# Kernel tuning notes

Measured on AMD Instinct MI355X. Metric: run time of the kernel, lower is better.

The kernel has to match this reference:

```python
import jax, jax.numpy as jnp
import numpy as np

B, L, N, C = 32, 12, 512, 2
UNITS, OUT_DIM, HORIZON, K, NUM_LAYERS = 64, 1, 12, 2, 2
M = 2 * K + 1  # 2 supports * K diffusion steps + identity


def _random_walk(adj):
    # adj: (B, N, N); D^-1 (adj + I)
    adj = adj + jnp.eye(adj.shape[1], dtype=adj.dtype)[None]
    d_inv = 1.0 / jnp.sum(adj, axis=2)
    d_inv = jnp.where(jnp.isinf(d_inv), 0.0, d_inv)
    return d_inv[:, :, None] * adj  # diag(d_inv) @ adj


def _gconv(x_in, state, supports, W, b):
    # x_in: (B, N*in), state: (B, N*units) -> (B, N*out)
    b_sz = x_in.shape[0]
    x = jnp.concatenate([x_in.reshape(b_sz, N, -1), state.reshape(b_sz, N, -1)], axis=2)
    f = x.shape[2]
    x0 = x
    xs = [x0]
    for A in supports:
        x1 = jnp.einsum('bij,bjf->bif', A, x0)
        xs.append(x1)
        for _ in range(2, K + 1):
            x2 = 2.0 * jnp.einsum('bij,bjf->bif', A, x1) - x0
            xs.append(x2)
            x1, x0 = x2, x1  # faithful to original code (x0 carries across supports)
    xcat = jnp.stack(xs, axis=0)              # (M, B, N, f)
    xcat = xcat.transpose(1, 2, 3, 0).reshape(b_sz * N, f * M)
    out = xcat @ W + b
    return out.reshape(b_sz, N * W.shape[1])


def _cell(inp, hx, supports, p):
    Wg, bg, Wc, bc = p
    gate = jax.nn.sigmoid(_gconv(inp, hx, supports, Wg, bg)).reshape(-1, N, 2 * UNITS)
    r = gate[..., :UNITS].reshape(-1, N * UNITS)
    u = gate[..., UNITS:].reshape(-1, N * UNITS)
    c = jnp.tanh(_gconv(inp, r * hx, supports, Wc, bc))
    return u * hx + (1.0 - u) * c


def setup_inputs() -> dict:
    key = jax.random.key(0)
    ks = iter(jax.random.split(key, 32))
    def nrm(shape, scale=0.1):
        return jax.random.normal(next(ks), shape, dtype=jnp.float32) * scale
    inp = {
        'history_data': jax.random.normal(next(ks), (B, L, N, C), dtype=jnp.float32),
        'hidden_states': jax.random.normal(next(ks), (B, N, 96), dtype=jnp.float32),
        'sampled_adj': jax.random.uniform(next(ks), (B, N, N), dtype=jnp.float32),
    }
    sizes = {'enc0': C + UNITS, 'enc1': 2 * UNITS, 'dec0': OUT_DIM + UNITS, 'dec1': 2 * UNITS}
    for name, isz in sizes.items():
        inp[name + '_Wg'] = nrm((isz * M, 2 * UNITS))
        inp[name + '_bg'] = jnp.ones((2 * UNITS,), jnp.float32)   # bias_start=1.0
        inp[name + '_Wc'] = nrm((isz * M, UNITS))
        inp[name + '_bc'] = jnp.zeros((UNITS,), jnp.float32)
    inp['proj_W'] = nrm((UNITS, OUT_DIM))
    inp['proj_b'] = jnp.zeros((OUT_DIM,), jnp.float32)
    inp['fc1_W'] = nrm((96, 256))
    inp['fc1_b'] = jnp.zeros((256,), jnp.float32)
    inp['fc2_W'] = nrm((256, 64))
    inp['fc2_b'] = jnp.zeros((64,), jnp.float32)
    return inp


def _forward(history_data, hidden_states, sampled_adj,
             enc0_Wg, enc0_bg, enc0_Wc, enc0_bc, enc1_Wg, enc1_bg, enc1_Wc, enc1_bc,
             dec0_Wg, dec0_bg, dec0_Wc, dec0_bc, dec1_Wg, dec1_bg, dec1_Wc, dec1_bc,
             proj_W, proj_b, fc1_W, fc1_b, fc2_W, fc2_b):
    supports = [_random_walk(sampled_adj), _random_walk(jnp.swapaxes(sampled_adj, -1, -2))]
    enc_params = [(enc0_Wg, enc0_bg, enc0_Wc, enc0_bc), (enc1_Wg, enc1_bg, enc1_Wc, enc1_bc)]
    dec_params = [(dec0_Wg, dec0_bg, dec0_Wc, dec0_bc), (dec1_Wg, dec1_bg, dec1_Wc, dec1_bc)]

    hist = jnp.transpose(history_data.reshape(B, L, N * C), (1, 0, 2))  # (L, B, N*C)

    def enc_step(h, x_t):
        out = x_t
        new_h = []
        for i, p in enumerate(enc_params):
            nh = _cell(out, h[i], supports, p)
            new_h.append(nh)
            out = nh
        return jnp.stack(new_h), None

    h0 = jnp.zeros((NUM_LAYERS, B, N * UNITS), dtype=hist.dtype)
    enc_h, _ = jax.lax.scan(enc_step, h0, hist)

    # fc_his on TSFormer hidden states, added to every encoder layer's hidden
    his = jax.nn.relu(jax.nn.relu(hidden_states @ fc1_W + fc1_b) @ fc2_W + fc2_b)  # (B, N, 64)
    enc_h = (enc_h.reshape(NUM_LAYERS, B, N, UNITS) + his[None]).reshape(NUM_LAYERS, B, N * UNITS)

    go = jnp.zeros((B, N * OUT_DIM), dtype=hist.dtype)

    def dec_step(carry, _):
        dec_in, h = carry
        out = dec_in
        new_h = []
        for i, p in enumerate(dec_params):
            nh = _cell(out, h[i], supports, p)
            new_h.append(nh)
            out = nh
        proj = (out.reshape(-1, UNITS) @ proj_W + proj_b).reshape(B, N * OUT_DIM)
        return (proj, jnp.stack(new_h)), proj

    _, outs = jax.lax.scan(dec_step, (go, enc_h), None, length=HORIZON)  # (L, B, N*OUT)
    return jnp.transpose(outs, (1, 2, 0))  # (B, N*OUT_DIM, HORIZON)


def reference(history_data, hidden_states, sampled_adj,
              enc0_Wg, enc0_bg, enc0_Wc, enc0_bc, enc1_Wg, enc1_bg, enc1_Wc, enc1_bc,
              dec0_Wg, dec0_bg, dec0_Wc, dec0_bc, dec1_Wg, dec1_bg, dec1_Wc, dec1_bc,
              proj_W, proj_b, fc1_W, fc1_b, fc2_W, fc2_b):
    return _forward(history_data, hidden_states, sampled_adj,
                    enc0_Wg, enc0_bg, enc0_Wc, enc0_bc, enc1_Wg, enc1_bg, enc1_Wc, enc1_bc,
                    dec0_Wg, dec0_bg, dec0_Wc, dec0_bc, dec1_Wg, dec1_bg, dec1_Wc, dec1_bc,
                    proj_W, proj_b, fc1_W, fc1_b, fc2_W, fc2_b)
```

## Files before the change

kernel.cpp:

```cpp
#include <hip/hip_runtime.h>
#include <stdint.h>
#include <string.h>
#include <math.h>


using bfrag = __attribute__((__ext_vector_type__(8))) short;
using accv  = __attribute__((__ext_vector_type__(4))) float;

#define DEVI static __device__ __forceinline__

DEVI float bf2f(short x) {
  union { unsigned u; float f; } v; v.u = ((unsigned)(unsigned short)x) << 16; return v.f;
}
DEVI short f2bf(float f) {
  union { float f; unsigned u; } v; v.f = f;
  unsigned r = v.u + 0x7FFFu + ((v.u >> 16) & 1u);
  return (short)(r >> 16);
}
DEVI float ldx(const void* p, long i, int f32) {
  return f32 ? ((const float*)p)[i] : bf2f(((const short*)p)[i]);
}
DEVI void gl16(const short* g, short* l) {
  __builtin_amdgcn_global_load_lds(
      (const __attribute__((address_space(1))) void*)g,
      (__attribute__((address_space(3))) void*)l, 16, 0, 0);
}
template<int N> DEVI void s_wait_vmcnt() {
  asm volatile("s_waitcnt vmcnt(%0)" :: "i"(N) : "memory");
}

struct GP {
  const short* A;  long sA;  int lda;
  const short* BT; long sBT; int ldbt;
  int K;
  short* C; long sC; int ldc;
  short* CT;
  const void* bias;
  const short* V0;
  const int* flg;
  int outDim, oshift;
  int mtiles;
  const float* h; float* hw; const float* u;
  short* xc; int inpOff;
  const short* wct; short* vtcout;
  short* xgs; int xgsOff;
  short* xch;
  short* nxg; short* nxc;
  const void* hsrc; long hoff;
  const void* prw; const void* prb; void* dout; int tstep;
  short* xo0; short* xo1;
};

template<int EPI, int BM, int BN, int BK, int THR, int SWZ, int PIPE, int PAIR = 0>
__global__ __launch_bounds__(THR)
void gemm_k(GP pa, GP pb) {
  constexpr int W    = THR / 64;
  constexpr int WROW = BM / 32;
  constexpr int WCOL = (W / WROW < 1) ? 1 : W / WROW;
  constexpr int NT   = BN / (16 * WCOL);
  constexpr int CH   = BK / 8;
  constexpr int AI   = (BM * CH) / THR;
  constexpr int BI   = (BN * CH) / THR;
  constexpr int LD   = AI + BI;
  constexpr int TB   = (BM + BN) * BK;
  __shared__ __align__(16) short lds[PIPE*TB];
  const int tid  = threadIdx.x;
  const int w    = tid >> 6;
  const int lane = tid & 63;
  const int quad = lane >> 4, l16 = lane & 15;
  const int rowW = (w % WROW) * 32;
  const int colW = (w / WROW) * (NT * 16);
  int lay = 0;
  if constexpr (PAIR) lay = blockIdx.z;
  const GP& p = lay ? pb : pa;
  int m0, n0, bz;
  if constexpr (SWZ == 1) {
    const int blk = blockIdx.x;
    bz = blk & 31;
    const int tile = blk >> 5;
    if (EPI == 4 && p.wct != nullptr && BN == 64) {
      m0 = (tile >> 1) * BM; n0 = (tile & 1) * BN;
    } else {
      m0 = (tile % p.mtiles) * BM;
      n0 = (tile / p.mtiles) * BN;
    }
  } else {
    m0 = blockIdx.x * BM; n0 = blockIdx.y * BN;
    bz = PAIR ? 0 : blockIdx.z;
  }

  const short* Ab = p.A  + (long)bz * p.sA + m0 * (long)p.lda;
  const short* Bb = p.BT + (long)bz * p.sBT + n0 * (long)p.ldbt;

  accv acc[2][NT];
#pragma unroll
  for (int i = 0; i < 2; i++)
#pragma unroll
    for (int j = 0; j < NT; j++) { accv z = {0.f,0.f,0.f,0.f}; acc[i][j] = z; }

  const short* asrc[AI]; int aoff[AI];
#pragma unroll
  for (int i = 0; i < AI; i++) {
    const int s = (w*AI + i)*64 + lane;
    const int r = s / CH, c = (s % CH) ^ (r & 7);
    asrc[i] = Ab + (long)r * p.lda + c*8;
    aoff[i] = (w*AI + i)*512;
  }
  const short* bsrc[BI]; int boff[BI];
#pragma unroll
  for (int i = 0; i < BI; i++) {
    const int s = (w*BI + i)*64 + lane;
    const int r = s / CH, c = (s % CH) ^ (r & 7);
    bsrc[i] = Bb + (long)r * p.ldbt + c*8;
    boff[i] = BM*BK + (w*BI + i)*512;
  }

  const int nIter = p.K / BK;
#pragma unroll
  for (int s = 0; s < PIPE-1; ++s) {
    if (s < nIter) {
      const int kk = s * BK;
#pragma unroll
      for (int i = 0; i < AI; i++) gl16(asrc[i] + kk, &lds[s*TB + aoff[i]]);
#pragma unroll
      for (int i = 0; i < BI; i++) gl16(bsrc[i] + kk, &lds[s*TB + boff[i]]);
    }
  }

  for (int it = 0; it < nIter; ++it) {
    const int bufO = (it & (PIPE-1)) * TB;
    if (it + PIPE - 1 < nIter) {
      const int nxt = ((it + PIPE - 1) & (PIPE-1)) * TB;
      const int kk = (it + PIPE - 1) * BK;
#pragma unroll
      for (int i = 0; i < AI; i++) gl16(asrc[i] + kk, &lds[nxt + aoff[i]]);
#pragma unroll
      for (int i = 0; i < BI; i++) gl16(bsrc[i] + kk, &lds[nxt + boff[i]]);
    }
    const int rem = nIter - 1 - it;
    if (rem >= PIPE-1) { s_wait_vmcnt<(PIPE-1)*LD>(); }
    else {
      if constexpr (PIPE >= 8) { if (rem == 6) s_wait_vmcnt<6*LD>(); }
      if constexpr (PIPE >= 7) { if (rem == 5) s_wait_vmcnt<5*LD>(); }
      if constexpr (PIPE >= 6) { if (rem == 4) s_wait_vmcnt<4*LD>(); }
      if constexpr (PIPE >= 5) { if (rem == 3) s_wait_vmcnt<3*LD>(); }
      if constexpr (PIPE >= 4) { if (rem == 2) s_wait_vmcnt<2*LD>(); }
      if (rem == 1) s_wait_vmcnt<1*LD>();
      else if (rem == 0) s_wait_vmcnt<0>();
    }
    asm volatile("s_barrier" ::: "memory");
#pragma unroll
    for (int ks = 0; ks < BK; ks += 32) {
      const int ch = (ks >> 3) + quad;
      bfrag fa[2];
#pragma unroll
      for (int rt = 0; rt < 2; rt++) {
        const int ar = rowW + rt*16 + l16;
        fa[rt] = *(const bfrag*)&lds[bufO + (ar*CH + (ch ^ (ar & 7))) * 8];
      }
#pragma unroll
      for (int nt = 0; nt < NT; nt++) {
        const int br = colW + nt*16 + l16;
        bfrag fb = *(const bfrag*)&lds[bufO + BM*BK + (br*CH + (ch ^ (br & 7))) * 8];
        acc[0][nt] = __builtin_amdgcn_mfma_f32_16x16x32_bf16(fa[0], fb, acc[0][nt], 0, 0, 0);
        acc[1][nt] = __builtin_amdgcn_mfma_f32_16x16x32_bf16(fa[1], fb, acc[1][nt], 0, 0, 0);
      }
    }
    asm volatile("s_barrier" ::: "memory");
  }

  int f32 = 0;
  if constexpr (EPI == 1 || EPI == 4 || EPI == 5) f32 = *p.flg;

  if constexpr (EPI == 0 || EPI == 1 || EPI == 2) {
#pragma unroll
    for (int rt = 0; rt < 2; rt++) {
      const int rbase = m0 + rowW + rt*16 + quad*4;
#pragma unroll
      for (int nt = 0; nt < NT; nt++) {
        const int cc = n0 + colW + nt*16 + l16;
#pragma unroll
        for (int e = 0; e < 4; e++) {
          float val = acc[rt][nt][e];
          if constexpr (EPI == 1) { val += ldx(p.bias, cc, f32); val = val > 0.f ? val : 0.f; }
          p.C[(long)bz * p.sC + (long)(rbase + e) * p.ldc + cc] = f2bf(val);
        }
      }
    }
  }
  if constexpr (EPI == 2 || EPI == 3) {
    __syncthreads();
#pragma unroll
    for (int rt = 0; rt < 2; rt++)
#pragma unroll
      for (int nt = 0; nt < NT; nt++)
#pragma unroll
        for (int e = 0; e < 4; e++)
          lds[(colW + nt*16 + l16)*136 + (rowW + rt*16 + quad*4 + e)] = f2bf(acc[rt][nt][e]);
    __syncthreads();
    const int c = tid >> 2, seg = tid & 3;
    const int cG = n0 + c;
    const short* sp = &lds[c*136 + seg*32];
    long dst;
    if constexpr (EPI == 3) {
      const int m  = cG >> p.oshift;
      const int o  = cG & (p.outDim - 1);
      const int bb = m0 >> 9;
      dst = ((long)((bb * p.outDim + o) * 5 + m) << 9) + (m0 & 511) + seg*32;
    } else {
      dst = (((long)bz << 9) + cG) * 512 + m0 + seg*32;
    }
    short* dp = p.CT + dst;
    *(bfrag*)(dp)      = *(const bfrag*)(sp);
    *(bfrag*)(dp + 8)  = *(const bfrag*)(sp + 8);
    *(bfrag*)(dp + 16) = *(const bfrag*)(sp + 16);
    *(bfrag*)(dp + 24) = *(const bfrag*)(sp + 24);
  }
  if constexpr (EPI == 4) {
#pragma unroll
    for (int rt = 0; rt < 2; rt++) {
      const int nb = m0 + rowW + rt*16 + quad*4;
#pragma unroll
      for (int nt = 0; nt < NT; nt++) {
        const int o = n0 + colW + nt*16 + l16;
        const float bv = ldx(p.bias, o, f32);
#pragma unroll
        for (int e = 0; e < 4; e++) {
          const int nn = nb + e;
          float val = acc[rt][nt][e] + bv +
                      bf2f(p.V0[(long)(bz * p.outDim + o) * 2560 + nn]);
          const float s = 1.f / (1.f + __expf(-val));
          const long bn = ((long)bz << 9) + nn;
          if (o < 64) p.xc[bn*128 + p.inpOff + o] = f2bf(s * p.h[(bn << 6) + o]);
          else        p.hw[(bn << 6) + (o - 64)] = s;
        }
      }
    }
    if (p.wct != nullptr && (BN == 128 || n0 == 0)) {
      s_wait_vmcnt<0>();
      __syncthreads();
      constexpr int AG2 = 16 / W;
      {
        const short* xrow = p.xc + ((long)bz*512 + m0)*128;
#pragma unroll
        for (int i = 0; i < AG2; i++) {
          const int s = (w*AG2 + i)*64 + lane;
          const int r = s >> 4, c = (s & 15) ^ (r & 7);
          gl16(xrow + (long)r*128 + c*8, &lds[(w*AG2 + i)*512]);
        }
      }
      constexpr int CW2 = W / 2;
      constexpr int NT2 = 64 / (16 * CW2);
      const int colW2 = (w >> 1) * (NT2 * 16);
      const int rowW2 = (w & 1) * 32;
      for (int ncb = 0; ncb < 5; ncb++) {
#pragma unroll
        for (int i = 0; i < AG2; i++) {
          const int s = (w*AG2 + i)*64 + lane;
          const int j = s >> 4, c = (s & 15) ^ (j & 7);
          const int cc = ncb*64 + j;
          const int mo = (cc % 5)*64 + cc/5;
          gl16(p.wct + (long)mo*128 + c*8, &lds[8192 + (w*AG2 + i)*512]);
        }
        s_wait_vmcnt<0>();
        asm volatile("s_barrier" ::: "memory");
        accv a2[2][NT2];
#pragma unroll
        for (int i2 = 0; i2 < 2; i2++)
#pragma unroll
          for (int j2 = 0; j2 < NT2; j2++) { accv z = {0.f,0.f,0.f,0.f}; a2[i2][j2] = z; }
#pragma unroll
        for (int k4 = 0; k4 < 4; k4++) {
          bfrag fa2[2];
#pragma unroll
          for (int rt = 0; rt < 2; rt++) {
            const int ar = rowW2 + rt*16 + l16;
            fa2[rt] = *(const bfrag*)&lds[(ar*16 + ((k4*4 + quad) ^ (ar & 7)))*8];
          }
#pragma unroll
          for (int nt = 0; nt < NT2; nt++) {
            const int jb = colW2 + nt*16 + l16;
            bfrag fb2 = *(const bfrag*)&lds[8192 + (jb*16 + ((k4*4 + quad) ^ (jb & 7)))*8];
            a2[0][nt] = __builtin_amdgcn_mfma_f32_16x16x32_bf16(fa2[0], fb2, a2[0][nt], 0, 0, 0);
            a2[1][nt] = __builtin_amdgcn_mfma_f32_16x16x32_bf16(fa2[1], fb2, a2[1][nt], 0, 0, 0);
          }
        }
#pragma unroll
        for (int rt = 0; rt < 2; rt++)
#pragma unroll
          for (int nt = 0; nt < NT2; nt++) {
            const int cc = ncb*64 + colW2 + nt*16 + l16;
            const long cbase = (((long)(bz*320 + cc)) << 9) + m0 + rowW2 + rt*16 + quad*4;
#pragma unroll
            for (int e = 0; e < 4; e++)
              p.vtcout[cbase + e] = f2bf(a2[rt][nt][e]);
          }
        asm volatile("s_barrier" ::: "memory");
      }
    }
  }
  if constexpr (EPI == 5) {
    float pacc[2][4] = {};
    float pwv[NT] = {};
    const bool doproj = (p.dout != nullptr);
    if (doproj) {
#pragma unroll
      for (int nt = 0; nt < NT; nt++) pwv[nt] = ldx(p.prw, colW + nt*16 + l16, f32);
    }
#pragma unroll
    for (int rt = 0; rt < 2; rt++) {
      const int nb = m0 + rowW + rt*16 + quad*4;
#pragma unroll
      for (int nt = 0; nt < NT; nt++) {
        const int o = n0 + colW + nt*16 + l16;
        const float bv = ldx(p.bias, o, f32);
#pragma unroll
        for (int e = 0; e < 4; e++) {
          const int nn = nb + e;
          float val = acc[rt][nt][e] + bv +
                      bf2f(p.V0[(long)(bz * p.outDim + o) * 2560 + nn]);
          const float cth = tanhf(val);
          const long bn = ((long)bz << 9) + nn;
          const long idx = bn*64 + o;
          const float uo = p.u[idx];
          const float hn = uo * p.h[idx] + (1.f - uo) * cth;
          p.hw[idx] = hn;
          pacc[rt][e] += hn * pwv[nt];
          const short hb = f2bf(hn);
          if (p.xgs) p.xgs[bn*128 + p.xgsOff + o] = hb;
          if (p.nxg) { p.nxg[bn*128 + o] = hb; p.nxc[bn*128 + o] = hb; }
          if (p.hsrc != nullptr && o < 2) {
            const short hv = f2bf(ldx(p.hsrc, p.hoff + (long)bz*12288 + (long)nn*2 + o, f32));
            p.xgs[bn*128 + o] = hv;
            p.xch[bn*128 + o] = hv;
          }
        }
      }
    }
    if (doproj) {
      __syncthreads();
      float* fl = (float*)lds;
#pragma unroll
      for (int rt = 0; rt < 2; rt++)
#pragma unroll
        for (int e = 0; e < 4; e++) {
          float v = pacc[rt][e];
          v += __shfl_xor(v, 1, 16);
          v += __shfl_xor(v, 2, 16);
          v += __shfl_xor(v, 4, 16);
          v += __shfl_xor(v, 8, 16);
          if (l16 == 0) fl[(rowW + rt*16 + quad*4 + e) * WCOL + (w / WROW)] = v;
        }
      __syncthreads();
      if (tid < BM) {
        float s = ldx(p.prb, 0, f32);
#pragma unroll
        for (int g = 0; g < WCOL; g++) s += fl[tid*WCOL + g];
        const long row = ((long)bz << 9) + m0 + tid;
        if (f32) ((float*)p.dout)[row*12 + p.tstep] = s;
        else     ((short*)p.dout)[row*12 + p.tstep] = f2bf(s);
        const short ob = f2bf(s);
        p.xo0[row*128] = ob;
        p.xo1[row*128] = ob;
      }
    }
  }
}


__global__ void detect_k(const short* bg0, int* flag) {
  if (threadIdx.x == 0 && blockIdx.x == 0)
    *flag = (bg0[0] == (short)0x3F80) ? 0 : 1;
}

__global__ void rowsum_inv(const void* adj, const int* flg, float* rsi) {
  const int f32 = *flg;
  const int wid  = (blockIdx.x * 256 + threadIdx.x) >> 6;
  const int lane = threadIdx.x & 63;
  const long base = (long)wid * 512;
  float s = 0.f;
  for (int j = lane; j < 512; j += 64) s += ldx(adj, base + j, f32);
  for (int off = 32; off > 0; off >>= 1) s += __shfl_down(s, off, 64);
  if (lane == 0) rsi[wid] = 1.f / (1.f + s);
}

__global__ void colsum_part(const void* adj, const int* flg, float* csum) {
  const int f32 = *flg;
  const int b = blockIdx.x >> 4, rc = blockIdx.x & 15;
  const int col = threadIdx.x;
  float s0 = 0.f, s1 = 0.f;
  const long base = (long)b * 262144 + (long)rc * 32 * 512;
  for (int r = 0; r < 32; r++) {
    s0 += ldx(adj, base + (long)r*512 + col, f32);
    s1 += ldx(adj, base + (long)r*512 + col + 256, f32);
  }
  atomicAdd(&csum[b*512 + col], s0);
  atomicAdd(&csum[b*512 + col + 256], s1);
}
__global__ void inv1p(float* v) {
  const int i = blockIdx.x * 256 + threadIdx.x;
  v[i] = 1.f / (1.f + v[i]);
}

__global__ __launch_bounds__(256)
void build_a(const void* adj, const int* flg, const float* rsi, const float* csi,
             short* Pbig, short* A1T, short* A2) {
  const int f32 = *flg;
  __shared__ __align__(16) float t[64 * 65];
  const int b = blockIdx.z, ti = blockIdx.x, tj = blockIdx.y;
  const int tid = threadIdx.x;
  const int r = tid >> 2, cs = (tid & 3) * 16;
  const long base = (long)b * 262144 + (long)(ti*64 + r) * 512 + tj*64 + cs;
#pragma unroll
  for (int j = 0; j < 16; j++) t[r*65 + cs + j] = ldx(adj, base + j, f32);
  __syncthreads();
  {
    const int gi = ti*64 + r;
    const float inv = rsi[b*512 + gi];
    short o[16];
#pragma unroll
    for (int j = 0; j < 16; j++) {
      const int gj = tj*64 + cs + j;
      o[j] = f2bf((t[r*65 + cs + j] + (gi == gj ? 1.f : 0.f)) * inv);
    }
    short* dp = Pbig + ((long)(b*512 + gi) << 11) + tj*64 + cs;
    bfrag v0 = {o[0],o[1],o[2],o[3],o[4],o[5],o[6],o[7]};
    bfrag v1 = {o[8],o[9],o[10],o[11],o[12],o[13],o[14],o[15]};
    *(bfrag*)dp = v0; *(bfrag*)(dp + 8) = v1;
  }
  {
    const int y = tj*64 + r;
    const float invc = csi[b*512 + y];
    short o1[16], o2[16];
#pragma unroll
    for (int j = 0; j < 16; j++) {
      const int x = ti*64 + cs + j;
      const float av = t[(cs + j)*65 + r];
      const float d = (x == y) ? 1.f : 0.f;
      o1[j] = f2bf((av + d) * rsi[b*512 + x]);
      o2[j] = f2bf((av + d) * invc);
    }
    short* d1 = A1T + ((long)(b*512 + y) << 9) + ti*64 + cs;
    short* d2 = A2  + ((long)(b*512 + y) << 9) + ti*64 + cs;
    bfrag a0 = {o1[0],o1[1],o1[2],o1[3],o1[4],o1[5],o1[6],o1[7]};
    bfrag a1 = {o1[8],o1[9],o1[10],o1[11],o1[12],o1[13],o1[14],o1[15]};
    bfrag b0 = {o2[0],o2[1],o2[2],o2[3],o2[4],o2[5],o2[6],o2[7]};
    bfrag b1 = {o2[8],o2[9],o2[10],o2[11],o2[12],o2[13],o2[14],o2[15]};
    *(bfrag*)d1 = a0; *(bfrag*)(d1 + 8) = a1;
    *(bfrag*)d2 = b0; *(bfrag*)(d2 + 8) = b1;
  }
}

__global__ void build_wcat(const void* W, const int* flg, short* WT, int f, int out) {
  const int f32 = *flg;
  const int i = blockIdx.x * 256 + threadIdx.x;
  if (i >= 5 * out * 128) return;
  const int feat = i & 127;
  const int mo = i >> 7;
  const int m = mo / out;
  const int o = mo - m * out;
  float v = 0.f;
  if (feat < f) {
    const long base = (long)feat * 5 * out;
    const float w0 = ldx(W, base + 0*out + o, f32);
    const float w1 = ldx(W, base + 1*out + o, f32);
    const float w2 = ldx(W, base + 2*out + o, f32);
    const float w3 = ldx(W, base + 3*out + o, f32);
    const float w4 = ldx(W, base + 4*out + o, f32);
    v = (m == 0) ? (w0 - w2) : (m == 1) ? (w1 - w4) : (m == 2) ? 2.f*w2
      : (m == 3) ? w3 : 2.f*w4;
  }
  WT[(long)mo * 128 + feat] = f2bf(v);
}

__global__ void build_fc1T(const void* W, const int* flg, short* WT) {
  const int f32 = *flg;
  const int i = blockIdx.x * 256 + threadIdx.x;
  const int o = i >> 7, k = i & 127;
  WT[i] = (k < 96) ? f2bf(ldx(W, (long)k*256 + o, f32)) : (short)0;
}
__global__ void build_fc2T(const void* W, const int* flg, short* WT) {
  const int f32 = *flg;
  const int i = blockIdx.x * 256 + threadIdx.x;
  const int o = i >> 8, k = i & 255;
  WT[i] = f2bf(ldx(W, (long)k*64 + o, f32));
}
__global__ void pack_hid(const void* hd, const int* flg, short* hp) {
  const int f32 = *flg;
  const int i = blockIdx.x * 256 + threadIdx.x;
  const int row = i >> 7, k = i & 127;
  hp[i] = (k < 96) ? f2bf(ldx(hd, (long)row*96 + k, f32)) : (short)0;
}

__global__ void seed_hist(const void* hist, const int* flg, short* Xg0, short* Xc0) {
  const int f32 = *flg;
  const int i = blockIdx.x * 256 + threadIdx.x;
  const int row = i >> 1, c = i & 1;
  const short v = f2bf(ldx(hist, (long)(row >> 9)*12288 + (long)(row & 511)*2 + c, f32));
  Xg0[(long)row*128 + c] = v;
  Xc0[(long)row*128 + c] = v;
}

__global__ void his_add(float* h0, float* h1, const short* his,
                        short* Xg0, short* Xc0, short* Xg1) {
  const int i = blockIdx.x * 256 + threadIdx.x;
  const int row = i >> 6, o = i & 63;
  const float v = bf2f(his[i]);
  const float a = h0[i] + v, b = h1[i] + v;
  h0[i] = a; h1[i] = b;
  Xg0[(long)row*128 + 1 + o]  = f2bf(a);
  Xg1[(long)row*128 + 64 + o] = f2bf(b);
  if (o == 0) { Xg0[(long)row*128] = 0; Xc0[(long)row*128] = 0; }
}

extern "C" void kernel_launch(void* const* d_in, const int* in_sizes, int n_in,
                              void* d_out, int out_size, void* d_ws, size_t ws_size,
                              hipStream_t stream) {
  (void)in_sizes; (void)n_in; (void)out_size;
  const void* hist   = d_in[0];
  const void* hidden = d_in[1];
  const void* adj    = d_in[2];
  const void* Wg[4] = {d_in[3], d_in[7],  d_in[11], d_in[15]};
  const void* bg[4] = {d_in[4], d_in[8],  d_in[12], d_in[16]};
  const void* Wc[4] = {d_in[5], d_in[9],  d_in[13], d_in[17]};
  const void* bc[4] = {d_in[6], d_in[10], d_in[14], d_in[18]};
  const void* projW = d_in[19];
  const void* projb = d_in[20];
  const void* fc1W  = d_in[21];
  const void* fc1b  = d_in[22];
  const void* fc2W  = d_in[23];
  const void* fc2b  = d_in[24];

  char* wp = (char*)d_ws;
  auto alloc = [&](size_t bytes) { char* r = wp; wp += (bytes + 255) & ~(size_t)255; return r; };
  short* Pbig = (short*)alloc(32ull*512*2048*2);
  float* ub   = (float*)alloc(16384ull*64*4);
  float* h0   = (float*)alloc(16384ull*64*4);
  float* h1   = (float*)alloc(16384ull*64*4);
  short* hisb = (short*)alloc(16384ull*64*2);
  short* wctg[4]; for (int i = 0; i < 4; i++) wctg[i] = (short*)alloc(640*128*2);
  short* wctc[4]; for (int i = 0; i < 4; i++) wctc[i] = (short*)alloc(320*128*2);
  float* rsi = (float*)alloc(16384*4);
  float* csi = (float*)alloc(16384*4);
  int*   flg = (int*)alloc(256);
  char* ubase = wp;
  short* hidp = (short*)ubase;
  short* mid  = (short*)(ubase + 4194304);
  short* fc1T = (short*)(ubase + 4194304 + 8388608);
  short* fc2T = (short*)(ubase + 4194304 + 8388608 + 65536);
  short* A1T  = (short*)ubase;
  short* A2   = (short*)(ubase + 16777216);
  short* P3T  = (short*)(ubase + 33554432);
  short* VTg0 = (short*)ubase;
  short* VTc0 = (short*)(ubase + 20971520);
  short* Xg0  = (short*)(ubase + 31457280);
  short* Xc0  = (short*)(ubase + 35651584);
  short* Xg1a = (short*)(ubase + 39845888);
  short* Xc1a = (short*)(ubase + 44040192);
  short* VTg1 = (short*)(ubase + 50331648);
  short* VTc1 = (short*)(ubase + 71303168);
  short* Xg1b = (short*)(ubase + 81788928);
  short* Xc1b = (short*)(ubase + 85983232);
  float* ub1  = (float*)(ubase + 90177536);
  const size_t need_serial = (size_t)(ubase - (char*)d_ws) + 50331648;
  const size_t need_pip    = (size_t)(ubase - (char*)d_ws) + 94371840;
  if (ws_size < need_serial) return;
  const bool pip = (ws_size >= need_pip);

  detect_k<<<1, 64, 0, stream>>>((const short*)bg[0], flg);
  hipMemsetAsync(h0, 0, 16384ull*64*4, stream);
  hipMemsetAsync(h1, 0, 16384ull*64*4, stream);

  const int fdim[4] = {66, 128, 65, 128};
  for (int i = 0; i < 4; i++) {
    build_wcat<<<320, 256, 0, stream>>>(Wg[i], flg, wctg[i], fdim[i], 128);
    build_wcat<<<160, 256, 0, stream>>>(Wc[i], flg, wctc[i], fdim[i], 64);
  }
  build_fc1T<<<128, 256, 0, stream>>>(fc1W, flg, fc1T);
  build_fc2T<<<64, 256, 0, stream>>>(fc2W, flg, fc2T);
  pack_hid<<<8192, 256, 0, stream>>>(hidden, flg, hidp);

  GP p;
  p = GP{}; p.A = hidp; p.lda = 128; p.BT = fc1T; p.ldbt = 128; p.K = 128;
  p.C = mid; p.ldc = 256; p.bias = fc1b; p.flg = flg;
  gemm_k<1,128,64,64,256,0,2><<<dim3(128, 4, 1), 256, 0, stream>>>(p, p);
  p = GP{}; p.A = mid; p.lda = 256; p.BT = fc2T; p.ldbt = 256; p.K = 256;
  p.C = hisb; p.ldc = 64; p.bias = fc2b; p.flg = flg;
  gemm_k<1,128,64,64,256,0,2><<<dim3(128, 1, 1), 256, 0, stream>>>(p, p);

  rowsum_inv<<<4096, 256, 0, stream>>>(adj, flg, rsi);
  hipMemsetAsync(csi, 0, 16384*4, stream);
  colsum_part<<<512, 256, 0, stream>>>(adj, flg, csi);
  inv1p<<<64, 256, 0, stream>>>(csi);
  build_a<<<dim3(8, 8, 32), 256, 0, stream>>>(adj, flg, rsi, csi, Pbig, A1T, A2);

  p = GP{}; p.A = Pbig; p.sA = 512*2048; p.lda = 2048;
  p.BT = A1T; p.sBT = 512*512; p.ldbt = 512; p.K = 512;
  p.C = Pbig + 512; p.sC = 512*2048; p.ldc = 2048; p.flg = flg;
  gemm_k<0,128,64,64,256,0,2><<<dim3(4, 8, 32), 256, 0, stream>>>(p, p);
  p = GP{}; p.A = A2; p.sA = 512*512; p.lda = 512;
  p.BT = A1T; p.sBT = 512*512; p.ldbt = 512; p.K = 512;
  p.C = Pbig + 1024; p.sC = 512*2048; p.ldc = 2048; p.CT = P3T; p.flg = flg;
  gemm_k<2,128,64,64,256,0,2><<<dim3(4, 8, 32), 256, 0, stream>>>(p, p);
  p = GP{}; p.A = A2; p.sA = 512*512; p.lda = 512;
  p.BT = P3T; p.sBT = 512*512; p.ldbt = 512; p.K = 512;
  p.C = Pbig + 1536; p.sC = 512*2048; p.ldc = 2048; p.flg = flg;
  gemm_k<0,128,64,64,256,0,2><<<dim3(4, 8, 32), 256, 0, stream>>>(p, p);

  hipMemsetAsync(Xg0, 0, 4ull*4194304, stream);
  seed_hist<<<128, 256, 0, stream>>>(hist, flg, Xg0, Xc0);

  auto run_cell = [&](int wi, int inpOff, float* hstate, short* XgL, short* XcL,
                      short* nxg, short* nxc, const void* hsrc, long hoff,
                      short* vtg, short* vtc, float* ubuf, void* dout, int tstep) {
    GP q;
    q = GP{}; q.A = XgL; q.lda = 128; q.BT = wctg[wi]; q.ldbt = 128; q.K = 128;
    q.CT = vtg; q.outDim = 128; q.oshift = 7; q.flg = flg;
    gemm_k<3,128,128,64,512,0,2><<<dim3(128, 5, 1), 512, 0, stream>>>(q, q);
    q = GP{}; q.A = Pbig; q.sA = 512*2048; q.lda = 2048;
    q.BT = vtg + 512; q.sBT = 128*2560; q.ldbt = 2560; q.K = 2048;
    q.V0 = vtg; q.outDim = 128; q.bias = bg[wi]; q.flg = flg; q.mtiles = 8;
    q.h = hstate; q.hw = ubuf; q.xc = XcL; q.inpOff = inpOff;
    q.wct = wctc[wi]; q.vtcout = vtc;
    gemm_k<4,64,64,64,256,1,4><<<dim3(512, 1, 1), 256, 0, stream>>>(q, q);
    q = GP{}; q.A = Pbig; q.sA = 512*2048; q.lda = 2048;
    q.BT = vtc + 512; q.sBT = 64*2560; q.ldbt = 2560; q.K = 2048;
    q.V0 = vtc; q.outDim = 64; q.bias = bc[wi]; q.flg = flg; q.mtiles = 16;
    q.h = hstate; q.hw = hstate; q.u = ubuf;
    q.xgs = XgL; q.xgsOff = inpOff; q.xch = XcL;
    q.nxg = nxg; q.nxc = nxc; q.hsrc = hsrc; q.hoff = hoff;
    q.prw = projW; q.prb = projb; q.dout = dout; q.tstep = tstep;
    q.xo0 = Xg0; q.xo1 = Xc0;
    gemm_k<5,32,64,64,256,1,4><<<dim3(512, 1, 1), 256, 0, stream>>>(q, q);
  };

  if (pip) {
    run_cell(0, 2, h0, Xg0, Xc0, Xg1a, Xc1a, hist, 1024, VTg0, VTc0, ub, nullptr, 0);
    for (int s = 1; s <= 11; s++) {
      short* XgR = ((s-1) & 1) ? Xg1b : Xg1a;
      short* XcR = ((s-1) & 1) ? Xc1b : Xc1a;
      short* XgW = (s & 1) ? Xg1b : Xg1a;
      short* XcW = (s & 1) ? Xc1b : Xc1a;
      GP qa, qb;
      qa = GP{}; qa.A = Xg0; qa.lda = 128; qa.BT = wctg[0]; qa.ldbt = 128; qa.K = 128;
      qa.CT = VTg0; qa.outDim = 128; qa.oshift = 7; qa.flg = flg;
      qb = qa; qb.A = XgR; qb.BT = wctg[1]; qb.CT = VTg1;
      gemm_k<3,128,128,64,512,0,2,1><<<dim3(128, 5, 2), 512, 0, stream>>>(qa, qb);
      qa = GP{}; qa.A = Pbig; qa.sA = 512*2048; qa.lda = 2048;
      qa.BT = VTg0 + 512; qa.sBT = 128*2560; qa.ldbt = 2560; qa.K = 2048;
      qa.V0 = VTg0; qa.outDim = 128; qa.bias = bg[0]; qa.flg = flg; qa.mtiles = 8;
      qa.h = h0; qa.hw = ub; qa.xc = Xc0; qa.inpOff = 2;
      qa.wct = wctc[0]; qa.vtcout = VTc0;
      qb = qa; qb.BT = VTg1 + 512; qb.V0 = VTg1; qb.bias = bg[1];
      qb.h = h1; qb.hw = ub1; qb.xc = XcR; qb.inpOff = 64;
      qb.wct = wctc[1]; qb.vtcout = VTc1;
      gemm_k<4,64,128,64,512,1,2,1><<<dim3(256, 1, 2), 512, 0, stream>>>(qa, qb);
      qa = GP{}; qa.A = Pbig; qa.sA = 512*2048; qa.lda = 2048;
      qa.BT = VTc0 + 512; qa.sBT = 64*2560; qa.ldbt = 2560; qa.K = 2048;
      qa.V0 = VTc0; qa.outDim = 64; qa.bias = bc[0]; qa.flg = flg; qa.mtiles = 8;
      qa.h = h0; qa.hw = h0; qa.u = ub;
      qa.xgs = Xg0; qa.xgsOff = 2; qa.xch = Xc0;
      qa.nxg = XgW; qa.nxc = XcW;
      qa.hsrc = (s < 11) ? hist : nullptr; qa.hoff = (long)(s + 1) * 1024;
      qb = qa; qb.BT = VTc1 + 512; qb.V0 = VTc1; qb.bias = bc[1];
      qb.h = h1; qb.hw = h1; qb.u = ub1;
      qb.xgs = XgW; qb.xgsOff = 64; qb.xch = nullptr;
      qb.nxg = nullptr; qb.nxc = nullptr; qb.hsrc = nullptr; qb.hoff = 0;
      gemm_k<5,64,64,64,256,1,4,1><<<dim3(256, 1, 2), 256, 0, stream>>>(qa, qb);
    }
    run_cell(1, 64, h1, Xg1b, Xc1b, nullptr, nullptr, nullptr, 0, VTg1, VTc1, ub1,
             nullptr, 0);
  } else {
    for (int t = 0; t < 12; t++) {
      run_cell(0, 2, h0, Xg0, Xc0, Xg1a, Xc1a,
               (t < 11) ? hist : nullptr, (long)(t + 1) * 1024, VTg0, VTc0, ub, nullptr, 0);
      run_cell(1, 64, h1, Xg1a, Xc1a, nullptr, nullptr, nullptr, 0, VTg0, VTc0, ub,
               nullptr, 0);
    }
  }

  his_add<<<4096, 256, 0, stream>>>(h0, h1, hisb, Xg0, Xc0, Xg1a);

  for (int t = 0; t < 12; t++) {
    run_cell(2, 1, h0, Xg0, Xc0, Xg1a, Xc1a, nullptr, 0, VTg0, VTc0, ub, nullptr, 0);
    run_cell(3, 64, h1, Xg1a, Xc1a, nullptr, nullptr, nullptr, 0, VTg0, VTc0, ub,
             d_out, t);
  }
}
```

Measured before the change: 3.060 ms.

## Fuse next cell's gate weight projection into candidate-epilogue kernel in decoder

```diff
diff --git a/kernel.cpp b/kernel.cpp
--- a/kernel.cpp
+++ b/kernel.cpp
@@ -49,6 +49,7 @@
   const void* hsrc; long hoff;
   const void* prw; const void* prb; void* dout; int tstep;
   short* xo0; short* xo1;
+  const short* g1s; const short* wgt; short* vtgout;
 };
 
 template<int EPI, int BM, int BN, int BK, int THR, int SWZ, int PIPE, int PAIR = 0>
@@ -362,6 +363,55 @@
         const short ob = f2bf(s);
         p.xo0[row*128] = ob;
         p.xo1[row*128] = ob;
+      }
+    }
+    if constexpr (BM == 32 && THR == 256) {
+      if (p.wgt != nullptr) {
+        s_wait_vmcnt<0>();
+        __syncthreads();
+        const short* xrow = p.g1s + ((long)bz*512 + m0)*128;
+#pragma unroll
+        for (int i = 0; i < 2; i++) {
+          const int s = (w*2 + i)*64 + lane;
+          const int r = s >> 4, c = (s & 15) ^ (r & 7);
+          gl16(xrow + (long)r*128 + c*8, &lds[(w*2 + i)*512]);
+        }
+        const int colg = (w >> 1) * 32;
+        const int rowg = (w & 1) * 16;
+        for (int ncb = 0; ncb < 10; ncb++) {
+#pragma unroll
+          for (int i = 0; i < 4; i++) {
+            const int s = (w*4 + i)*64 + lane;
+            const int j = s >> 4, c = (s & 15) ^ (j & 7);
+            const int cc = ncb*64 + j;
+            const int mo = (cc % 5)*128 + cc/5;
+            gl16(p.wgt + (long)mo*128 + c*8, &lds[4096 + (w*4 + i)*512]);
+          }
+          s_wait_vmcnt<0>();
+          asm volatile("s_barrier" ::: "memory");
+          accv a3[2];
+          { accv z = {0.f,0.f,0.f,0.f}; a3[0] = z; a3[1] = z; }
+#pragma unroll
+          for (int k4 = 0; k4 < 4; k4++) {
+            const int ar = rowg + l16;
+            bfrag fa3 = *(const bfrag*)&lds[(ar*16 + ((k4*4 + quad) ^ (ar & 7)))*8];
+#pragma unroll
+            for (int nt = 0; nt < 2; nt++) {
+              const int jb = colg + nt*16 + l16;
+              bfrag fb3 = *(const bfrag*)&lds[4096 + (jb*16 + ((k4*4 + quad) ^ (jb & 7)))*8];
+              a3[nt] = __builtin_amdgcn_mfma_f32_16x16x32_bf16(fa3, fb3, a3[nt], 0, 0, 0);
+            }
+          }
+#pragma unroll
+          for (int nt = 0; nt < 2; nt++) {
+            const int cc = ncb*64 + colg + nt*16 + l16;
+            const long cbase = (((long)(bz*640 + cc)) << 9) + m0 + rowg + quad*4;
+#pragma unroll
+            for (int e = 0; e < 4; e++)
+              p.vtgout[cbase + e] = f2bf(a3[nt][e]);
+          }
+          asm volatile("s_barrier" ::: "memory");
+        }
       }
     }
   }
@@ -612,11 +662,14 @@
 
   auto run_cell = [&](int wi, int inpOff, float* hstate, short* XgL, short* XcL,
                       short* nxg, short* nxc, const void* hsrc, long hoff,
-                      short* vtg, short* vtc, float* ubuf, void* dout, int tstep) {
+                      short* vtg, short* vtc, float* ubuf, void* dout, int tstep,
+                      bool skipG1g, const short* g1s, const short* g1w, short* g1o) {
     GP q;
-    q = GP{}; q.A = XgL; q.lda = 128; q.BT = wctg[wi]; q.ldbt = 128; q.K = 128;
-    q.CT = vtg; q.outDim = 128; q.oshift = 7; q.flg = flg;
-    gemm_k<3,128,128,64,512,0,2><<<dim3(128, 5, 1), 512, 0, stream>>>(q, q);
+    if (!skipG1g) {
+      q = GP{}; q.A = XgL; q.lda = 128; q.BT = wctg[wi]; q.ldbt = 128; q.K = 128;
+      q.CT = vtg; q.outDim = 128; q.oshift = 7; q.flg = flg;
+      gemm_k<3,128,128,64,512,0,2><<<dim3(128, 5, 1), 512, 0, stream>>>(q, q);
+    }
     q = GP{}; q.A = Pbig; q.sA = 512*2048; q.lda = 2048;
     q.BT = vtg + 512; q.sBT = 128*2560; q.ldbt = 2560; q.K = 2048;
     q.V0 = vtg; q.outDim = 128; q.bias = bg[wi]; q.flg = flg; q.mtiles = 8;
@@ -631,11 +684,13 @@
     q.nxg = nxg; q.nxc = nxc; q.hsrc = hsrc; q.hoff = hoff;
     q.prw = projW; q.prb = projb; q.dout = dout; q.tstep = tstep;
     q.xo0 = Xg0; q.xo1 = Xc0;
+    q.g1s = g1s; q.wgt = g1w; q.vtgout = g1o;
     gemm_k<5,32,64,64,256,1,4><<<dim3(512, 1, 1), 256, 0, stream>>>(q, q);
   };
 
   if (pip) {
-    run_cell(0, 2, h0, Xg0, Xc0, Xg1a, Xc1a, hist, 1024, VTg0, VTc0, ub, nullptr, 0);
+    run_cell(0, 2, h0, Xg0, Xc0, Xg1a, Xc1a, hist, 1024, VTg0, VTc0, ub, nullptr, 0,
+             false, nullptr, nullptr, nullptr);
     for (int s = 1; s <= 11; s++) {
       short* XgR = ((s-1) & 1) ? Xg1b : Xg1a;
       short* XcR = ((s-1) & 1) ? Xc1b : Xc1a;
@@ -669,21 +724,29 @@
       gemm_k<5,64,64,64,256,1,4,1><<<dim3(256, 1, 2), 256, 0, stream>>>(qa, qb);
     }
     run_cell(1, 64, h1, Xg1b, Xc1b, nullptr, nullptr, nullptr, 0, VTg1, VTc1, ub1,
-             nullptr, 0);
+             nullptr, 0, false, nullptr, nullptr, nullptr);
   } else {
     for (int t = 0; t < 12; t++) {
       run_cell(0, 2, h0, Xg0, Xc0, Xg1a, Xc1a,
-               (t < 11) ? hist : nullptr, (long)(t + 1) * 1024, VTg0, VTc0, ub, nullptr, 0);
+               (t < 11) ? hist : nullptr, (long)(t + 1) * 1024, VTg0, VTc0, ub, nullptr, 0,
+               false, nullptr, nullptr, nullptr);
       run_cell(1, 64, h1, Xg1a, Xc1a, nullptr, nullptr, nullptr, 0, VTg0, VTc0, ub,
-               nullptr, 0);
+               nullptr, 0, false, nullptr, nullptr, nullptr);
     }
   }
 
   his_add<<<4096, 256, 0, stream>>>(h0, h1, hisb, Xg0, Xc0, Xg1a);
 
+  {
+    GP qi{}; qi.A = Xg0; qi.lda = 128; qi.BT = wctg[2]; qi.ldbt = 128; qi.K = 128;
+    qi.CT = VTg0; qi.outDim = 128; qi.oshift = 7; qi.flg = flg;
+    gemm_k<3,128,128,64,512,0,2><<<dim3(128, 5, 1), 512, 0, stream>>>(qi, qi);
+  }
   for (int t = 0; t < 12; t++) {
-    run_cell(2, 1, h0, Xg0, Xc0, Xg1a, Xc1a, nullptr, 0, VTg0, VTc0, ub, nullptr, 0);
+    run_cell(2, 1, h0, Xg0, Xc0, Xg1a, Xc1a, nullptr, 0, VTg0, VTc0, ub, nullptr, 0,
+             true, Xg1a, wctg[3], VTg0);
     run_cell(3, 64, h1, Xg1a, Xc1a, nullptr, nullptr, nullptr, 0, VTg0, VTc0, ub,
-             d_out, t);
-  }
-}
+             d_out, t,
+             true, Xg0, (t < 11) ? wctg[2] : nullptr, VTg0);
+  }
+}
```

Result: faster. 2.970 ms (-2.9%).
